# Kernel optimization log

Measured on AMD Instinct MI355X. Metric: run time of the kernel, lower is better.

## Reference

```python
import jax, jax.numpy as jnp
import numpy as np

K_SIZE = 5  # local window size (odd, SAME padding, stride 1)


def _local_attn(x_main, x_ref, W_main, W_ref, k_size=K_SIZE):
    # 1x1 convs == per-pixel channel matmuls
    cm = jnp.einsum('bhwc,cd->bhwd', x_main, W_main)  # query  [B,H,W,C']
    cr = jnp.einsum('bhwc,cd->bhwd', x_ref, W_ref)    # keys   [B,H,W,C']
    pad = (k_size - 1) // 2
    B, H, W, C = cr.shape
    crp = jnp.pad(cr, ((0, 0), (pad, pad), (pad, pad), (0, 0)))
    # score for each of the k*k offsets: dot(query, shifted key) per pixel.
    # Avoids materializing the [B,H,W,k*k,C] patch tensor.
    scores = [
        jnp.einsum('bhwc,bhwc->bhw', cm, crp[:, i:i + H, j:j + W, :])
        for i in range(k_size) for j in range(k_size)
    ]
    # the layer concatenates the query itself as the last "key" (self score)
    scores.append(jnp.einsum('bhwc,bhwc->bhw', cm, cm))
    attn = jnp.stack(scores, axis=-1)  # [B,H,W,k*k+1]
    return jax.nn.softmax(attn, axis=-1)


def setup_inputs() -> dict:
    key = jax.random.key(0)
    k1, k2, k3, k4 = jax.random.split(key, 4)
    B, H, W, C = 4, 128, 128, 64
    Ci = 64  # intermediate_dim
    return {
        'x_main': jax.random.normal(k1, (B, H, W, C), jnp.float32),
        'x_ref': jax.random.normal(k2, (B, H, W, C), jnp.float32),
        'W_main': jax.random.normal(k3, (C, Ci), jnp.float32) * (2.0 / C) ** 0.5,
        'W_ref': jax.random.normal(k4, (C, Ci), jnp.float32) * (2.0 / C) ** 0.5,
    }


def reference(x_main, x_ref, W_main, W_ref):
    return _local_attn(x_main, x_ref, W_main, W_ref)
```

## Files before the change

### kernel.cpp

```cpp
#include <hip/hip_runtime.h>
#include <math.h>

#define HDIM 128
#define WDIM 128
#define CDIM 64
#define BDIM 4
#define NPIX (BDIM * HDIM * WDIM)

__global__ void conv1x1_kernel(const float* __restrict__ xm,
                               const float* __restrict__ xr,
                               const float* __restrict__ Wm,
                               const float* __restrict__ Wr,
                               float* __restrict__ outm,
                               float* __restrict__ outr) {
    const float* x; const float* Wg; float* out;
    if (blockIdx.y == 0) { x = xm; Wg = Wm; out = outm; }
    else                 { x = xr; Wg = Wr; out = outr; }

    __shared__ float Ws[CDIM][CDIM];
    __shared__ float xs[CDIM][132];

    const int t = threadIdx.x;
    const int pxbase = blockIdx.x * 128;

    {
        const float4* Wg4 = (const float4*)Wg;
        float4* Ws4 = (float4*)&Ws[0][0];
        #pragma unroll
        for (int i = 0; i < 4; ++i) Ws4[t + 256 * i] = Wg4[t + 256 * i];
    }
    #pragma unroll
    for (int i = 0; i < 8; ++i) {
        int L  = t + 256 * i;
        int px = L >> 4;
        int c4 = L & 15;
        float4 v = *(const float4*)&x[(size_t)(pxbase + px) * CDIM + 4 * c4];
        xs[4 * c4 + 0][px] = v.x;
        xs[4 * c4 + 1][px] = v.y;
        xs[4 * c4 + 2][px] = v.z;
        xs[4 * c4 + 3][px] = v.w;
    }
    __syncthreads();

    const int dg = t & 7;
    const int pg = t >> 3;

    float acc[4][8];
    #pragma unroll
    for (int i = 0; i < 4; ++i)
        #pragma unroll
        for (int j = 0; j < 8; ++j) acc[i][j] = 0.f;

    #pragma unroll 16
    for (int c = 0; c < CDIM; ++c) {
        float4 xv = *(const float4*)&xs[c][pg * 4];
        float4 w0 = *(const float4*)&Ws[c][dg * 8];
        float4 w1 = *(const float4*)&Ws[c][dg * 8 + 4];
        float xa[4] = {xv.x, xv.y, xv.z, xv.w};
        float wa[8] = {w0.x, w0.y, w0.z, w0.w, w1.x, w1.y, w1.z, w1.w};
        #pragma unroll
        for (int i = 0; i < 4; ++i)
            #pragma unroll
            for (int j = 0; j < 8; ++j)
                acc[i][j] = fmaf(xa[i], wa[j], acc[i][j]);
    }

    #pragma unroll
    for (int i = 0; i < 4; ++i) {
        int px = pxbase + pg * 4 + i;
        float4 o0 = {acc[i][0], acc[i][1], acc[i][2], acc[i][3]};
        float4 o1 = {acc[i][4], acc[i][5], acc[i][6], acc[i][7]};
        *(float4*)&out[(size_t)px * CDIM + dg * 8]     = o0;
        *(float4*)&out[(size_t)px * CDIM + dg * 8 + 4] = o1;
    }
}

#define TILE_W 16
#define TILE_H 8
#define HALO_W 20
#define HALO_H 12
#define NHALO (HALO_W * HALO_H)
#define PSTRIDE 68

__global__ __launch_bounds__(256, 1)
void attn_tiled_kernel(const float* __restrict__ cm,
                       const float* __restrict__ cr,
                       float* __restrict__ out) {
    __shared__ float crs[NHALO * PSTRIDE];

    const int t   = threadIdx.x;
    const int tx0 = blockIdx.x * TILE_W;
    const int ty0 = blockIdx.y * TILE_H;
    const int b   = blockIdx.z;

    #pragma unroll
    for (int it = 0; it < 15; ++it) {
        int L   = t + 256 * it;
        int pix = L >> 4;
        int q   = L & 15;
        int hy  = pix / HALO_W;
        int hx  = pix - hy * HALO_W;
        int gy  = ty0 + hy - 2, gx = tx0 + hx - 2;
        float4 v = make_float4(0.f, 0.f, 0.f, 0.f);
        if (gy >= 0 && gy < HDIM && gx >= 0 && gx < WDIM) {
            size_t gp = ((size_t)b * HDIM + gy) * WDIM + gx;
            v = *(const float4*)&cr[gp * CDIM + 4 * q];
        }
        *(float4*)&crs[pix * PSTRIDE + 4 * q] = v;
    }
    __syncthreads();

    const int pl = t >> 1;
    const int cg = t & 1;
    const int lx = pl & (TILE_W - 1);
    const int ly = pl >> 4;
    const size_t gpx = ((size_t)b * HDIM + ty0 + ly) * WDIM + tx0 + lx;

    float4 qv[8];
    {
        const float4* cmp = (const float4*)&cm[gpx * CDIM + cg * 32];
        #pragma unroll
        for (int m = 0; m < 8; ++m) qv[m] = cmp[m];
    }

    float s[26];
    #pragma unroll
    for (int k = 0; k < 25; ++k) {
        const int i = k / 5, j = k % 5;
        const int p = (ly + i) * HALO_W + (lx + j);
        const float4* kp = (const float4*)&crs[p * PSTRIDE + cg * 32];
        float acc = 0.f;
        #pragma unroll
        for (int m = 0; m < 8; ++m) {
            float4 v = kp[m];
            acc = fmaf(qv[m].x, v.x, acc);
            acc = fmaf(qv[m].y, v.y, acc);
            acc = fmaf(qv[m].z, v.z, acc);
            acc = fmaf(qv[m].w, v.w, acc);
        }
        s[k] = acc;
    }
    {
        float acc = 0.f;
        #pragma unroll
        for (int m = 0; m < 8; ++m) {
            float4 v = qv[m];
            acc = fmaf(v.x, v.x, acc);
            acc = fmaf(v.y, v.y, acc);
            acc = fmaf(v.z, v.z, acc);
            acc = fmaf(v.w, v.w, acc);
        }
        s[25] = acc;
    }

    #pragma unroll
    for (int k = 0; k < 26; ++k) s[k] += __shfl_xor(s[k], 1);

    float mx = s[0];
    #pragma unroll
    for (int k = 1; k < 26; ++k) mx = fmaxf(mx, s[k]);
    float sum = 0.f;
    #pragma unroll
    for (int k = 0; k < 26; ++k) { s[k] = __expf(s[k] - mx); sum += s[k]; }
    const float inv = 1.f / sum;

    float* op = &out[gpx * 26 + cg * 13];
    if (cg == 0) {
        #pragma unroll
        for (int k = 0; k < 13; ++k) op[k] = s[k] * inv;
    } else {
        #pragma unroll
        for (int k = 0; k < 13; ++k) op[k] = s[13 + k] * inv;
    }
}

extern "C" void kernel_launch(void* const* d_in, const int* in_sizes, int n_in,
                              void* d_out, int out_size, void* d_ws, size_t ws_size,
                              hipStream_t stream) {
    const float* xm = (const float*)d_in[0];
    const float* xr = (const float*)d_in[1];
    const float* Wm = (const float*)d_in[2];
    const float* Wr = (const float*)d_in[3];
    float* outp = (float*)d_out;

    float* cm = (float*)d_ws;
    float* cr = cm + (size_t)NPIX * CDIM;

    dim3 g1(NPIX / 128, 2);
    conv1x1_kernel<<<g1, 256, 0, stream>>>(xm, xr, Wm, Wr, cm, cr);

    dim3 g2(WDIM / TILE_W, HDIM / TILE_H, BDIM);
    attn_tiled_kernel<<<g2, 256, 0, stream>>>(cm, cr, outp);
}
```

Before: 107.1 us.

## Compute 1x1 conv with split-bf16 MFMA instead of FP32 FMA

Replaces the FP32 FMA projection GEMM with MFMA bf16 16x16x32 instructions, splitting each float into hi and lo bf16 parts and running three products to keep near-FP32 accuracy. Each wave handles four 16-pixel tiles, loading activations straight from global memory into registers, and the grid shrinks to 256x2 blocks. This aims to move the conv's compute onto the matrix cores. In exchange it adds conversion work, fewer blocks, and uncoalesced scalar output stores.

```diff
diff --git a/kernel.cpp b/kernel.cpp
--- a/kernel.cpp
+++ b/kernel.cpp
@@ -7,71 +7,113 @@
 #define BDIM 4
 #define NPIX (BDIM * HDIM * WDIM)
 
-__global__ void conv1x1_kernel(const float* __restrict__ xm,
-                               const float* __restrict__ xr,
-                               const float* __restrict__ Wm,
-                               const float* __restrict__ Wr,
-                               float* __restrict__ outm,
-                               float* __restrict__ outr) {
+typedef short bf16x8 __attribute__((ext_vector_type(8)));
+typedef float f32x4  __attribute__((ext_vector_type(4)));
+
+__device__ __forceinline__ void split_bf16(float f, short& hi, short& lo) {
+    unsigned u = __float_as_uint(f);
+    hi = (short)(u >> 16);
+    float hf = __uint_as_float(u & 0xffff0000u);
+    float l  = f - hf;
+    lo = (short)(__float_as_uint(l) >> 16);
+}
+
+__global__ __launch_bounds__(256, 1)
+void conv1x1_mfma_kernel(const float* __restrict__ xm,
+                         const float* __restrict__ xr,
+                         const float* __restrict__ Wm,
+                         const float* __restrict__ Wr,
+                         float* __restrict__ outm,
+                         float* __restrict__ outr) {
     const float* x; const float* Wg; float* out;
     if (blockIdx.y == 0) { x = xm; Wg = Wm; out = outm; }
     else                 { x = xr; Wg = Wr; out = outr; }
 
-    __shared__ float Ws[CDIM][CDIM];
-    __shared__ float xs[CDIM][132];
-
+    __shared__ float Wsh[CDIM * CDIM];
     const int t = threadIdx.x;
-    const int pxbase = blockIdx.x * 128;
-
     {
         const float4* Wg4 = (const float4*)Wg;
-        float4* Ws4 = (float4*)&Ws[0][0];
+        float4* Ws4 = (float4*)Wsh;
         #pragma unroll
         for (int i = 0; i < 4; ++i) Ws4[t + 256 * i] = Wg4[t + 256 * i];
     }
-    #pragma unroll
-    for (int i = 0; i < 8; ++i) {
-        int L  = t + 256 * i;
-        int px = L >> 4;
-        int c4 = L & 15;
-        float4 v = *(const float4*)&x[(size_t)(pxbase + px) * CDIM + 4 * c4];
-        xs[4 * c4 + 0][px] = v.x;
-        xs[4 * c4 + 1][px] = v.y;
-        xs[4 * c4 + 2][px] = v.z;
-        xs[4 * c4 + 3][px] = v.w;
-    }
     __syncthreads();
 
-    const int dg = t & 7;
-    const int pg = t >> 3;
-
-    float acc[4][8];
-    #pragma unroll
-    for (int i = 0; i < 4; ++i)
-        #pragma unroll
-        for (int j = 0; j < 8; ++j) acc[i][j] = 0.f;
-
-    #pragma unroll 16
-    for (int c = 0; c < CDIM; ++c) {
-        float4 xv = *(const float4*)&xs[c][pg * 4];
-        float4 w0 = *(const float4*)&Ws[c][dg * 8];
-        float4 w1 = *(const float4*)&Ws[c][dg * 8 + 4];
-        float xa[4] = {xv.x, xv.y, xv.z, xv.w};
-        float wa[8] = {w0.x, w0.y, w0.z, w0.w, w1.x, w1.y, w1.z, w1.w};
-        #pragma unroll
-        for (int i = 0; i < 4; ++i)
-            #pragma unroll
-            for (int j = 0; j < 8; ++j)
-                acc[i][j] = fmaf(xa[i], wa[j], acc[i][j]);
-    }
-
-    #pragma unroll
-    for (int i = 0; i < 4; ++i) {
-        int px = pxbase + pg * 4 + i;
-        float4 o0 = {acc[i][0], acc[i][1], acc[i][2], acc[i][3]};
-        float4 o1 = {acc[i][4], acc[i][5], acc[i][6], acc[i][7]};
-        *(float4*)&out[(size_t)px * CDIM + dg * 8]     = o0;
-        *(float4*)&out[(size_t)px * CDIM + dg * 8 + 4] = o1;
+    const int lane = t & 63;
+    const int wv   = t >> 6;
+    const int m    = lane & 15;
+    const int quad = lane >> 4;
+
+    bf16x8 Bhi[2][4], Blo[2][4];
+    #pragma unroll
+    for (int ks = 0; ks < 2; ++ks) {
+        #pragma unroll
+        for (int nt = 0; nt < 4; ++nt) {
+            #pragma unroll
+            for (int j = 0; j < 8; ++j) {
+                float f = Wsh[(ks * 32 + quad * 8 + j) * CDIM + nt * 16 + m];
+                short hi, lo; split_bf16(f, hi, lo);
+                Bhi[ks][nt][j] = hi;
+                Blo[ks][nt][j] = lo;
+            }
+        }
+    }
+
+    const int tbase = (blockIdx.x * 4 + wv) * 4;
+
+    float4 pa[4][4];
+    #pragma unroll
+    for (int it = 0; it < 4; ++it) {
+        const float* ap = x + ((size_t)((tbase + it) * 16 + m)) * CDIM + quad * 8;
+        pa[it][0] = *(const float4*)(ap);
+        pa[it][1] = *(const float4*)(ap + 4);
+        pa[it][2] = *(const float4*)(ap + 32);
+        pa[it][3] = *(const float4*)(ap + 36);
+    }
+
+    #pragma unroll
+    for (int it = 0; it < 4; ++it) {
+        bf16x8 Ahi[2], Alo[2];
+        #pragma unroll
+        for (int ks = 0; ks < 2; ++ks) {
+            float fv[8];
+            float4 p = pa[it][2 * ks], q = pa[it][2 * ks + 1];
+            fv[0] = p.x; fv[1] = p.y; fv[2] = p.z; fv[3] = p.w;
+            fv[4] = q.x; fv[5] = q.y; fv[6] = q.z; fv[7] = q.w;
+            #pragma unroll
+            for (int j = 0; j < 8; ++j) {
+                short hi, lo; split_bf16(fv[j], hi, lo);
+                Ahi[ks][j] = hi;
+                Alo[ks][j] = lo;
+            }
+        }
+
+        f32x4 acc[4];
+        #pragma unroll
+        for (int nt = 0; nt < 4; ++nt) {
+            acc[nt][0] = 0.f; acc[nt][1] = 0.f;
+            acc[nt][2] = 0.f; acc[nt][3] = 0.f;
+        }
+        #pragma unroll
+        for (int ks = 0; ks < 2; ++ks) {
+            #pragma unroll
+            for (int nt = 0; nt < 4; ++nt) {
+                acc[nt] = __builtin_amdgcn_mfma_f32_16x16x32_bf16(
+                              Ahi[ks], Bhi[ks][nt], acc[nt], 0, 0, 0);
+                acc[nt] = __builtin_amdgcn_mfma_f32_16x16x32_bf16(
+                              Ahi[ks], Blo[ks][nt], acc[nt], 0, 0, 0);
+                acc[nt] = __builtin_amdgcn_mfma_f32_16x16x32_bf16(
+                              Alo[ks], Bhi[ks][nt], acc[nt], 0, 0, 0);
+            }
+        }
+
+        float* op = out + ((size_t)((tbase + it) * 16 + quad * 4)) * CDIM + m;
+        #pragma unroll
+        for (int nt = 0; nt < 4; ++nt) {
+            #pragma unroll
+            for (int r = 0; r < 4; ++r)
+                op[(size_t)r * CDIM + nt * 16] = acc[nt][r];
+        }
     }
 }
 
@@ -120,7 +162,7 @@
     {
         const float4* cmp = (const float4*)&cm[gpx * CDIM + cg * 32];
         #pragma unroll
-        for (int m = 0; m < 8; ++m) qv[m] = cmp[m];
+        for (int mq = 0; mq < 8; ++mq) qv[mq] = cmp[mq];
     }
 
     float s[26];
@@ -131,20 +173,20 @@
         const float4* kp = (const float4*)&crs[p * PSTRIDE + cg * 32];
         float acc = 0.f;
         #pragma unroll
-        for (int m = 0; m < 8; ++m) {
-            float4 v = kp[m];
-            acc = fmaf(qv[m].x, v.x, acc);
-            acc = fmaf(qv[m].y, v.y, acc);
-            acc = fmaf(qv[m].z, v.z, acc);
-            acc = fmaf(qv[m].w, v.w, acc);
+        for (int mq = 0; mq < 8; ++mq) {
+            float4 v = kp[mq];
+            acc = fmaf(qv[mq].x, v.x, acc);
+            acc = fmaf(qv[mq].y, v.y, acc);
+            acc = fmaf(qv[mq].z, v.z, acc);
+            acc = fmaf(qv[mq].w, v.w, acc);
         }
         s[k] = acc;
     }
     {
         float acc = 0.f;
         #pragma unroll
-        for (int m = 0; m < 8; ++m) {
-            float4 v = qv[m];
+        for (int mq = 0; mq < 8; ++mq) {
+            float4 v = qv[mq];
             acc = fmaf(v.x, v.x, acc);
             acc = fmaf(v.y, v.y, acc);
             acc = fmaf(v.z, v.z, acc);
@@ -186,8 +228,8 @@
     float* cm = (float*)d_ws;
     float* cr = cm + (size_t)NPIX * CDIM;
 
-    dim3 g1(NPIX / 128, 2);
-    conv1x1_kernel<<<g1, 256, 0, stream>>>(xm, xr, Wm, Wr, cm, cr);
+    dim3 g1(256, 2);
+    conv1x1_mfma_kernel<<<g1, 256, 0, stream>>>(xm, xr, Wm, Wr, cm, cr);
 
     dim3 g2(WDIM / TILE_W, HDIM / TILE_H, BDIM);
     attn_tiled_kernel<<<g2, 256, 0, stream>>>(cm, cr, outp);
```

After: 99.07 us. 1.08x faster.
